# Kernel tuning notes

Hardware: AMD Instinct MI355X
Metric: run time of the kernel (lower is better)

Reference implementation:

```python
import jax, jax.numpy as jnp
import numpy as np

B, S, D, H = 2, 2048, 1024, 16
DK = D // H


def setup_inputs() -> dict:
    key = jax.random.key(0)
    ks = jax.random.split(key, 6)
    scale = 1.0 / np.sqrt(D)
    return {
        "x": jax.random.normal(ks[0], (B, S, D), dtype=jnp.float32),
        "q": jax.random.normal(ks[1], (B, S, D), dtype=jnp.float32),
        "k": jax.random.normal(ks[2], (B, S, D), dtype=jnp.float32),
        "v": jax.random.normal(ks[3], (B, S, D), dtype=jnp.float32),
        "mask": jnp.ones((B, 1, S, S), dtype=jnp.int32),
        "Wq": jax.random.normal(ks[4], (D, D), dtype=jnp.float32) * scale,
        "Wo": jax.random.normal(ks[5], (D, D), dtype=jnp.float32) * scale,
    }


def reference(x, q, k, v, mask, Wq, Wo):
    b = x.shape[0]
    # NOTE: source projects q, k, v ALL through Wq (Wk/Wv unused in forward).
    def proj(t):
        # [b, s, D] -> [b, H, s, DK]   (nn.Linear: t @ W.T)
        return (t @ Wq.T).reshape(b, -1, H, DK).transpose(0, 2, 1, 3)

    query, key_, value = proj(q), proj(k), proj(v)
    # [b, H, Sq, Sk]
    scores = jnp.einsum("bhqd,bhkd->bhqk", query, key_) / np.sqrt(DK)
    scores = jnp.where(mask == 0, jnp.float32(1e-9), scores)
    attn = jax.nn.softmax(scores, axis=-1)
    out = jnp.einsum("bhqk,bhkd->bhqd", attn, value)  # [b, H, Sq, DK]
    out = out.transpose(0, 2, 1, 3).reshape(b, -1, D)
    return out @ Wo.T
```

## Files before the change

### kernel.cpp

```cpp
#include <hip/hip_runtime.h>

#define SEQ  2048
#define DDIM 1024
#define NH   16
#define DK   64

typedef _Float16 half8  __attribute__((ext_vector_type(8)));
typedef _Float16 half4v __attribute__((ext_vector_type(4)));
typedef _Float16 half2v __attribute__((ext_vector_type(2)));
typedef float    floatx4 __attribute__((ext_vector_type(4)));
typedef float    floatx16 __attribute__((ext_vector_type(16)));
typedef unsigned uint4v __attribute__((ext_vector_type(4)));

__device__ __forceinline__ float fast_exp2(float x) {
#if __has_builtin(__builtin_amdgcn_exp2f)
  return __builtin_amdgcn_exp2f(x);
#else
  return exp2f(x);
#endif
}

__device__ __forceinline__ void pl32swap(unsigned a, unsigned b,
                                         unsigned& x, unsigned& y, int hi) {
#if __has_builtin(__builtin_amdgcn_permlane32_swap)
  auto r = __builtin_amdgcn_permlane32_swap(a, b, false, false);
  x = r[0];
  y = r[1];
#else
  unsigned sa = (unsigned)__shfl_xor((int)a, 32, 64);
  unsigned sb = (unsigned)__shfl_xor((int)b, 32, 64);
  x = hi ? sb : a;
  y = hi ? b : sa;
#endif
}

__device__ __forceinline__ void gload16(const _Float16* g, _Float16* l) {
  __builtin_amdgcn_global_load_lds(
      (const __attribute__((address_space(1))) unsigned int*)(const void*)g,
      (__attribute__((address_space(3))) unsigned int*)(void*)l, 16, 0, 0);
}

template <int NR, int NW>
__device__ __forceinline__ void stage_w(const _Float16* __restrict__ src,
                                        int row0, int stride, int k0,
                                        _Float16* dst, int wl, int l) {
  constexpr int RPW = NR / NW;
  const int cg = (l & 7) ^ (l >> 3);
  const _Float16* gbase = src + k0 + cg * 8;
#pragma unroll
  for (int i = 0; i < RPW / 8; ++i) {
    int rl = wl * RPW + i * 8;
    gload16(gbase + (long)(row0 + rl + (l >> 3)) * stride, dst + rl * 64);
  }
}

template <int NR>
__device__ __forceinline__ void stage_gl(const _Float16* __restrict__ src,
                                         int row0, int stride, int k0,
                                         _Float16* dst) {
  stage_w<NR, 4>(src, row0, stride, k0, dst, threadIdx.x >> 6,
                 threadIdx.x & 63);
}

__global__ __launch_bounds__(256) void cvt_kernel(
    const float* __restrict__ q, const float* __restrict__ k,
    const float* __restrict__ v, const float* __restrict__ Wq,
    const float* __restrict__ Wo, _Float16* __restrict__ ws) {
  long t = (long)blockIdx.x * 256 + threadIdx.x;
  long base = t * 4;
  const float* src;
  long off;
  if (base < 12582912L) {
    int which = (int)(base >> 22);
    src = which == 0 ? q : (which == 1 ? k : v);
    off = base & 4194303L;
  } else if (base < 13631488L) {
    src = Wq; off = base - 12582912L;
  } else {
    src = Wo; off = base - 13631488L;
  }
  float4 f = *(const float4*)(src + off);
  half4v h;
  h[0] = (_Float16)f.x; h[1] = (_Float16)f.y;
  h[2] = (_Float16)f.z; h[3] = (_Float16)f.w;
  *(half4v*)(ws + base) = h;
}

__device__ __forceinline__ void gemm16_gl(
    const _Float16* __restrict__ A, const _Float16* __restrict__ B,
    int m0, int n0, _Float16* As, _Float16* Bs, floatx4 (&acc)[4][4]) {
  const int tid = threadIdx.x;
  const int lane = tid & 63, w = tid >> 6;
  const int wm = w >> 1, wn = w & 1;
  const int quad = lane >> 4, l15 = lane & 15;

#pragma unroll
  for (int i = 0; i < 4; ++i)
#pragma unroll
    for (int j = 0; j < 4; ++j)
#pragma unroll
      for (int r = 0; r < 4; ++r) acc[i][j][r] = 0.f;

  stage_gl<128>(A, m0, 1024, 0, As);
  stage_gl<128>(B, n0, 1024, 0, Bs);
  __syncthreads();

  for (int kt = 0; kt < 16; ++kt) {
    _Float16* Ap = As + (kt & 1) * 8192;
    _Float16* Bp = Bs + (kt & 1) * 8192;
    if (kt < 15) {
      stage_gl<128>(A, m0, 1024, (kt + 1) * 64, As + ((kt + 1) & 1) * 8192);
      stage_gl<128>(B, n0, 1024, (kt + 1) * 64, Bs + ((kt + 1) & 1) * 8192);
    }
#pragma unroll
    for (int kc = 0; kc < 2; ++kc) {
      half8 af[4], bf[4];
#pragma unroll
      for (int i = 0; i < 4; ++i) {
        int row = wm * 64 + i * 16 + l15;
        af[i] = *(const half8*)(Ap + row * 64 + (((kc * 4 + quad) ^ (row & 7)) * 8));
      }
#pragma unroll
      for (int j = 0; j < 4; ++j) {
        int row = wn * 64 + j * 16 + l15;
        bf[j] = *(const half8*)(Bp + row * 64 + (((kc * 4 + quad) ^ (row & 7)) * 8));
      }
#pragma unroll
      for (int i = 0; i < 4; ++i)
#pragma unroll
        for (int j = 0; j < 4; ++j)
          acc[i][j] = __builtin_amdgcn_mfma_f32_16x16x32_f16(af[i], bf[j],
                                                             acc[i][j], 0, 0, 0);
    }
    __syncthreads();
  }
}

__global__ __launch_bounds__(256) void proj_gemm(
    const _Float16* __restrict__ qkv16, const _Float16* __restrict__ w16,
    _Float16* __restrict__ Qp, _Float16* __restrict__ Kp,
    _Float16* __restrict__ Vt) {
  __shared__ __align__(16) _Float16 smem[32768];
  _Float16* As = smem;
  _Float16* Bs = smem + 16384;
  const int bid = (blockIdx.x & 7) * 96 + (blockIdx.x >> 3);
  const int lane = threadIdx.x & 63, w = threadIdx.x >> 6;
  const int wm = w >> 1, wn = w & 1;
  const int quad = lane >> 4, l15 = lane & 15;
  floatx4 acc[4][4];

  if (bid < 512) {
    const int m0 = (bid >> 3) * 128, n0 = (bid & 7) * 128;
    gemm16_gl(qkv16, w16, m0, n0, As, Bs, acc);
#pragma unroll
    for (int i = 0; i < 4; ++i)
#pragma unroll
      for (int j = 0; j < 4; ++j)
#pragma unroll
        for (int r = 0; r < 4; ++r) {
          int m = m0 + wm * 64 + i * 16 + quad * 4 + r;
          int n = n0 + wn * 64 + j * 16 + l15;
          int seq = m & 4095;
          int b = seq >> 11, s = seq & 2047, h = n >> 6, dk = n & 63;
          long bh = b * NH + h;
          float val = acc[i][j][r];
          if (m < 4096)
            Qp[(bh * SEQ + s) * DK + dk] = (_Float16)(val * 0.180336880f);
          else
            Kp[(bh * SEQ + s) * DK + dk] = (_Float16)val;
        }
  } else {
    const int local = bid - 512;
    const int m0 = (local >> 5) * 128;
    const int n0 = (local & 31) * 128;
    gemm16_gl(w16, qkv16 + 8388608L, m0, n0, As, Bs, acc);
#pragma unroll
    for (int i = 0; i < 4; ++i)
#pragma unroll
      for (int j = 0; j < 4; ++j)
#pragma unroll
        for (int r = 0; r < 4; ++r) {
          int m = m0 + wm * 64 + i * 16 + quad * 4 + r;
          int n = n0 + wn * 64 + j * 16 + l15;
          int h = m >> 6, dk = m & 63, b = n >> 11, s = n & 2047;
          Vt[(((long)b * NH + h) * DK + dk) * SEQ + s] = (_Float16)acc[i][j][r];
        }
  }
}

__global__ __launch_bounds__(256) void out_gemm(
    const _Float16* __restrict__ Aa, const _Float16* __restrict__ Bw,
    float* __restrict__ C) {
  __shared__ __align__(16) _Float16 smem[32768];
  _Float16* As = smem;
  _Float16* Bs = smem + 16384;
  const int bid = (blockIdx.x & 7) * 32 + (blockIdx.x >> 3);
  const int m0 = (bid >> 3) * 128, n0 = (bid & 7) * 128;
  floatx4 acc[4][4];
  gemm16_gl(Aa, Bw, m0, n0, As, Bs, acc);

  const int lane = threadIdx.x & 63, w = threadIdx.x >> 6;
  const int wm = w >> 1, wn = w & 1;
  const int quad = lane >> 4, l15 = lane & 15;
#pragma unroll
  for (int i = 0; i < 4; ++i)
#pragma unroll
    for (int j = 0; j < 4; ++j)
#pragma unroll
      for (int r = 0; r < 4; ++r) {
        int m = m0 + wm * 64 + i * 16 + quad * 4 + r;
        int n = n0 + wn * 64 + j * 16 + l15;
        C[(long)m * 1024 + n] = acc[i][j][r];
      }
}

__global__ __launch_bounds__(512, 2) void attn_kernel(
    const _Float16* __restrict__ Qp, const _Float16* __restrict__ Kp,
    const _Float16* __restrict__ Vt, _Float16* __restrict__ Oa) {
  __shared__ __align__(16) _Float16 smem[32768];
  const int tid = threadIdx.x;
  const int lane = tid & 63, w = tid >> 6;
  const int g = w >> 2, wl = w & 3;
  const int l31 = lane & 31, hi = lane >> 5;
  const int swz = (blockIdx.x & 7) * 64 + (blockIdx.x >> 3);
  const int bh = swz >> 4;
  const int q0 = (swz & 15) * 128;
  const _Float16* Qb = Qp + (long)bh * (SEQ * DK);
  const _Float16* Kb = Kp + (long)bh * (SEQ * DK) + (long)g * 1024 * DK;
  const _Float16* Vb = Vt + (long)bh * (DK * SEQ);
  const int vc0 = g * 1024;
  _Float16* KVg = smem + g * 16384;

  const int qrow = wl * 32 + l31;

  half8 qf[4];
  {
    stage_w<128, 8>(Qb, q0, DK, 0, smem, w, lane);
    __syncthreads();
#pragma unroll
    for (int dks = 0; dks < 4; ++dks) {
      int c = dks * 2 + hi;
      qf[dks] = *(const half8*)(smem + qrow * 64 + ((c ^ (qrow & 7)) * 8));
    }
    __syncthreads();
  }
  stage_w<64, 4>(Kb, 0, DK, 0, KVg, wl, lane);
  stage_w<64, 4>(Vb, 0, SEQ, vc0, KVg + 8192, wl, lane);
  __syncthreads();

  floatx16 Oacc[2];
#pragma unroll
  for (int dt = 0; dt < 2; ++dt)
#pragma unroll
    for (int r = 0; r < 16; ++r) Oacc[dt][r] = 0.f;
  float den = 0.f;

  for (int lt = 0; lt < 16; ++lt) {
    _Float16* Kcur = KVg + (lt & 1) * 4096;
    _Float16* Vcur = KVg + 8192 + (lt & 1) * 4096;
    if (lt < 15) {
      stage_w<64, 4>(Kb, (lt + 1) * 64, DK, 0,
                     KVg + ((lt + 1) & 1) * 4096, wl, lane);
      stage_w<64, 4>(Vb, 0, SEQ, vc0 + (lt + 1) * 64,
                     KVg + 8192 + ((lt + 1) & 1) * 4096, wl, lane);
    }

#pragma unroll
    for (int kt2 = 0; kt2 < 2; ++kt2) {
      floatx16 S;
#pragma unroll
      for (int r = 0; r < 16; ++r) S[r] = 0.f;
      const int krow = kt2 * 32 + l31;
      __builtin_amdgcn_s_setprio(1);
#pragma unroll
      for (int dks = 0; dks < 4; ++dks) {
        int c = dks * 2 + hi;
        half8 kf = *(const half8*)(Kcur + krow * 64 + ((c ^ (krow & 7)) * 8));
        S = __builtin_amdgcn_mfma_f32_32x32x16_f16(kf, qf[dks], S, 0, 0, 0);
      }
      __builtin_amdgcn_s_setprio(0);

      unsigned d[8];
#pragma unroll
      for (int i = 0; i < 8; ++i) {
        float e0 = fast_exp2(S[2 * i]);
        float e1 = fast_exp2(S[2 * i + 1]);
        den += e0 + e1;
        d[i] = __builtin_bit_cast(unsigned,
                                  __builtin_amdgcn_cvt_pkrtz(e0, e1));
      }
      half8 p[2];
#pragma unroll
      for (int hseg = 0; hseg < 2; ++hseg) {
        unsigned x0, y0, x1, y1;
        pl32swap(d[hseg * 4 + 0], d[hseg * 4 + 2], x0, y0, hi);
        pl32swap(d[hseg * 4 + 1], d[hseg * 4 + 3], x1, y1, hi);
        uint4v u;
        u[0] = x0; u[1] = x1; u[2] = y0; u[3] = y1;
        p[hseg] = __builtin_bit_cast(half8, u);
      }

      __builtin_amdgcn_s_setprio(1);
#pragma unroll
      for (int dt = 0; dt < 2; ++dt) {
        int drow = dt * 32 + l31;
#pragma unroll
        for (int kk = 0; kk < 2; ++kk) {
          int c = (kt2 * 2 + kk) * 2 + hi;
          half8 vf = *(const half8*)(Vcur + drow * 64 + ((c ^ (drow & 7)) * 8));
          Oacc[dt] = __builtin_amdgcn_mfma_f32_32x32x16_f16(vf, p[kk],
                                                            Oacc[dt], 0, 0, 0);
        }
      }
      __builtin_amdgcn_s_setprio(0);
    }
    __syncthreads();
  }

  den += __shfl_xor(den, 32, 64);

  float* exch = (float*)(smem + 8192);
  float* denx = (float*)(smem + 25600);
  if (g == 1) {
#pragma unroll
    for (int dt = 0; dt < 2; ++dt)
#pragma unroll
      for (int i = 0; i < 4; ++i) {
        floatx4 v;
#pragma unroll
        for (int r = 0; r < 4; ++r) v[r] = Oacc[dt][4 * i + r];
        *(floatx4*)(exch + qrow * 68 + dt * 32 + 8 * i + 4 * hi) = v;
      }
    if (hi == 0) denx[qrow] = den;
  }
  __syncthreads();

  if (g == 0) {
    float inv = __builtin_amdgcn_rcpf(den + denx[qrow]);
#pragma unroll
    for (int dt = 0; dt < 2; ++dt)
#pragma unroll
      for (int i = 0; i < 4; ++i) {
        floatx4 o1 = *(const floatx4*)(exch + qrow * 68 + dt * 32 + 8 * i +
                                       4 * hi);
        half4v o;
#pragma unroll
        for (int r = 0; r < 4; ++r)
          o[r] = (_Float16)((Oacc[dt][4 * i + r] + o1[r]) * inv);
        int c8 = dt * 4 + i;
        *(half4v*)(smem + qrow * 64 + ((c8 ^ (qrow & 7)) * 8) + 4 * hi) = o;
      }
  }
  __syncthreads();

  const int b = bh >> 4, h = bh & 15;
  const int qloc = tid >> 2, part = tid & 3;
#pragma unroll
  for (int cc = 0; cc < 2; ++cc) {
    int c8 = part + cc * 4;
    half8 val = *(const half8*)(smem + qloc * 64 + ((c8 ^ (qloc & 7)) * 8));
    *(half8*)(Oa + ((long)b * SEQ + q0 + qloc) * DDIM + h * DK + c8 * 8) = val;
  }
}

extern "C" void kernel_launch(void* const* d_in, const int* in_sizes, int n_in,
                              void* d_out, int out_size, void* d_ws,
                              size_t ws_size, hipStream_t stream) {
  const float* q  = (const float*)d_in[1];
  const float* k  = (const float*)d_in[2];
  const float* v  = (const float*)d_in[3];
  const float* Wq = (const float*)d_in[5];
  const float* Wo = (const float*)d_in[6];
  float* out = (float*)d_out;

  _Float16* ws     = (_Float16*)d_ws;
  _Float16* qkv16  = ws;
  _Float16* wq16   = ws + 12582912;
  _Float16* wo16   = ws + 13631488;
  _Float16* Qp     = ws + 14680064;
  _Float16* Kp     = ws + 18874368;
  _Float16* Vt     = ws + 23068672;
  _Float16* attn16 = ws + 27262976;

  cvt_kernel<<<14336, 256, 0, stream>>>(q, k, v, Wq, Wo, ws);
  proj_gemm<<<768, 256, 0, stream>>>(qkv16, wq16, Qp, Kp, Vt);
  attn_kernel<<<512, 512, 0, stream>>>(Qp, Kp, Vt, attn16);
  out_gemm<<<256, 256, 0, stream>>>(attn16, wo16, out);
}
```

Baseline: 224.3 us.

## Software-pipeline attention so PV MFMAs of previous tile overlap current softmax

Restructures the attention inner loop so the P·V matrix multiply for the previous key tile is issued alongside the QK^T MFMAs of the current tile, while the exp/convert/permlane work for the current tile follows. V gets a triple-buffered shared-memory ring and P fragments are double-buffered in registers, with a final drain step after the loop. The goal is to hide the softmax ALU latency behind matrix-core work. In exchange, shared memory per block grows from 64KB to 80KB and register pressure rises, which may hurt occupancy at two blocks per CU.

```diff
diff --git a/kernel.cpp b/kernel.cpp
--- a/kernel.cpp
+++ b/kernel.cpp
@@ -217,7 +217,7 @@
 __global__ __launch_bounds__(512, 2) void attn_kernel(
     const _Float16* __restrict__ Qp, const _Float16* __restrict__ Kp,
     const _Float16* __restrict__ Vt, _Float16* __restrict__ Oa) {
-  __shared__ __align__(16) _Float16 smem[32768];
+  __shared__ __align__(16) _Float16 smem[40960];
   const int tid = threadIdx.x;
   const int lane = tid & 63, w = tid >> 6;
   const int g = w >> 2, wl = w & 3;
@@ -229,7 +229,9 @@
   const _Float16* Kb = Kp + (long)bh * (SEQ * DK) + (long)g * 1024 * DK;
   const _Float16* Vb = Vt + (long)bh * (DK * SEQ);
   const int vc0 = g * 1024;
-  _Float16* KVg = smem + g * 16384;
+  _Float16* KVg = smem + g * 20480;
+  _Float16* Ks  = KVg;
+  _Float16* Vs  = KVg + 8192;
 
   const int qrow = wl * 32 + l31;
 
@@ -244,8 +246,8 @@
     }
     __syncthreads();
   }
-  stage_w<64, 4>(Kb, 0, DK, 0, KVg, wl, lane);
-  stage_w<64, 4>(Vb, 0, SEQ, vc0, KVg + 8192, wl, lane);
+  stage_w<64, 4>(Kb, 0, DK, 0, Ks, wl, lane);
+  stage_w<64, 4>(Vb, 0, SEQ, vc0, Vs, wl, lane);
   __syncthreads();
 
   floatx16 Oacc[2];
@@ -255,14 +257,16 @@
     for (int r = 0; r < 16; ++r) Oacc[dt][r] = 0.f;
   float den = 0.f;
 
-  for (int lt = 0; lt < 16; ++lt) {
-    _Float16* Kcur = KVg + (lt & 1) * 4096;
-    _Float16* Vcur = KVg + 8192 + (lt & 1) * 4096;
+  _Float16 *Vp = Vs + 8192, *Vc = Vs, *Vn = Vs + 4096;
+
+  half8 pbA[4], pbB[4];
+
+  auto iter = [&](int lt, half8* pprev, half8* pcur) {
+    _Float16* Kcur = Ks + (lt & 1) * 4096;
     if (lt < 15) {
-      stage_w<64, 4>(Kb, (lt + 1) * 64, DK, 0,
-                     KVg + ((lt + 1) & 1) * 4096, wl, lane);
-      stage_w<64, 4>(Vb, 0, SEQ, vc0 + (lt + 1) * 64,
-                     KVg + 8192 + ((lt + 1) & 1) * 4096, wl, lane);
+      stage_w<64, 4>(Kb, (lt + 1) * 64, DK, 0, Ks + ((lt + 1) & 1) * 4096,
+                     wl, lane);
+      stage_w<64, 4>(Vb, 0, SEQ, vc0 + (lt + 1) * 64, Vn, wl, lane);
     }
 
 #pragma unroll
@@ -277,6 +281,19 @@
         int c = dks * 2 + hi;
         half8 kf = *(const half8*)(Kcur + krow * 64 + ((c ^ (krow & 7)) * 8));
         S = __builtin_amdgcn_mfma_f32_32x32x16_f16(kf, qf[dks], S, 0, 0, 0);
+      }
+      if (lt > 0) {
+#pragma unroll
+        for (int dt = 0; dt < 2; ++dt) {
+          int drow = dt * 32 + l31;
+#pragma unroll
+          for (int kk = 0; kk < 2; ++kk) {
+            int c = (kt2 * 2 + kk) * 2 + hi;
+            half8 vf = *(const half8*)(Vp + drow * 64 + ((c ^ (drow & 7)) * 8));
+            Oacc[dt] = __builtin_amdgcn_mfma_f32_32x32x16_f16(
+                vf, pprev[kt2 * 2 + kk], Oacc[dt], 0, 0, 0);
+          }
+        }
       }
       __builtin_amdgcn_s_setprio(0);
 
@@ -289,7 +306,6 @@
         d[i] = __builtin_bit_cast(unsigned,
                                   __builtin_amdgcn_cvt_pkrtz(e0, e1));
       }
-      half8 p[2];
 #pragma unroll
       for (int hseg = 0; hseg < 2; ++hseg) {
         unsigned x0, y0, x1, y1;
@@ -297,30 +313,38 @@
         pl32swap(d[hseg * 4 + 1], d[hseg * 4 + 3], x1, y1, hi);
         uint4v u;
         u[0] = x0; u[1] = x1; u[2] = y0; u[3] = y1;
-        p[hseg] = __builtin_bit_cast(half8, u);
-      }
-
-      __builtin_amdgcn_s_setprio(1);
-#pragma unroll
-      for (int dt = 0; dt < 2; ++dt) {
-        int drow = dt * 32 + l31;
-#pragma unroll
-        for (int kk = 0; kk < 2; ++kk) {
-          int c = (kt2 * 2 + kk) * 2 + hi;
-          half8 vf = *(const half8*)(Vcur + drow * 64 + ((c ^ (drow & 7)) * 8));
-          Oacc[dt] = __builtin_amdgcn_mfma_f32_32x32x16_f16(vf, p[kk],
-                                                            Oacc[dt], 0, 0, 0);
-        }
-      }
-      __builtin_amdgcn_s_setprio(0);
+        pcur[kt2 * 2 + hseg] = __builtin_bit_cast(half8, u);
+      }
     }
     __syncthreads();
-  }
+    _Float16* t = Vp; Vp = Vc; Vc = Vn; Vn = t;
+  };
+
+  for (int lt = 0; lt < 16; lt += 2) {
+    iter(lt, pbB, pbA);
+    iter(lt + 1, pbA, pbB);
+  }
+
+  __builtin_amdgcn_s_setprio(1);
+#pragma unroll
+  for (int dt = 0; dt < 2; ++dt) {
+    int drow = dt * 32 + l31;
+#pragma unroll
+    for (int kc = 0; kc < 4; ++kc) {
+      int c = kc * 2 + hi;
+      half8 vf = *(const half8*)(Vp + drow * 64 + ((c ^ (drow & 7)) * 8));
+      Oacc[dt] = __builtin_amdgcn_mfma_f32_32x32x16_f16(vf, pbB[kc],
+                                                        Oacc[dt], 0, 0, 0);
+    }
+  }
+  __builtin_amdgcn_s_setprio(0);
 
   den += __shfl_xor(den, 32, 64);
-
-  float* exch = (float*)(smem + 8192);
-  float* denx = (float*)(smem + 25600);
+  __syncthreads();
+
+  float* exch = (float*)smem;
+  float* denx = (float*)(smem + 17408);
+  _Float16* Ot = smem + 17920;
   if (g == 1) {
 #pragma unroll
     for (int dt = 0; dt < 2; ++dt)
@@ -348,7 +372,7 @@
         for (int r = 0; r < 4; ++r)
           o[r] = (_Float16)((Oacc[dt][4 * i + r] + o1[r]) * inv);
         int c8 = dt * 4 + i;
-        *(half4v*)(smem + qrow * 64 + ((c8 ^ (qrow & 7)) * 8) + 4 * hi) = o;
+        *(half4v*)(Ot + qrow * 64 + ((c8 ^ (qrow & 7)) * 8) + 4 * hi) = o;
       }
   }
   __syncthreads();
@@ -358,7 +382,7 @@
 #pragma unroll
   for (int cc = 0; cc < 2; ++cc) {
     int c8 = part + cc * 4;
-    half8 val = *(const half8*)(smem + qloc * 64 + ((c8 ^ (qloc & 7)) * 8));
+    half8 val = *(const half8*)(Ot + qloc * 64 + ((c8 ^ (qloc & 7)) * 8));
     *(half8*)(Oa + ((long)b * SEQ + q0 + qloc) * DDIM + h * DK + c8 * 8) = val;
   }
 }
```

Measured after the change: 226.5 us. About the same (+1.0%).
